# Kernel tuning notes

Hardware: AMD Instinct MI355X
Metric: run time of the kernel (lower is better)

Reference implementation:

```python
import jax, jax.numpy as jnp
import numpy as np

B, T, D_MODEL, N_HEADS = 2, 2048, 1024, 16
HEAD_DIM = D_MODEL // N_HEADS          # 64
CODE_SIZE = HEAD_DIM // 4              # 16


def setup_inputs() -> dict:
    key = jax.random.key(0)
    k1, k2, k3, k4 = jax.random.split(key, 4)
    x = jax.random.normal(k1, (B, T, D_MODEL), dtype=jnp.float32)
    # nn.Linear weights (out_features, in_features), fan-in init scale
    w_qkv = jax.random.normal(k2, (3 * D_MODEL, D_MODEL), dtype=jnp.float32) / np.sqrt(D_MODEL)
    w_out = jax.random.normal(k3, (D_MODEL, D_MODEL), dtype=jnp.float32) / np.sqrt(D_MODEL)
    fc_code = jax.random.normal(k4, (1, N_HEADS, CODE_SIZE, HEAD_DIM), dtype=jnp.float32)
    return {"x": x, "w_qkv": w_qkv, "w_out": w_out, "fc_code": fc_code}


def reference(x, w_qkv, w_out, fc_code):
    Bx, Tx, _ = x.shape
    scale = HEAD_DIM ** (-0.5)
    qkv = x @ w_qkv.T                                   # (B,T,3*d_model)
    # split_heads with Hs=head_dim on 3*d_model -> (B, 3*nH, T, Hs), then chunk on head axis
    qkv = qkv.reshape(Bx, Tx, 3 * N_HEADS, HEAD_DIM).transpose(0, 2, 1, 3)
    q, k, v = qkv[:, :N_HEADS], qkv[:, N_HEADS:2 * N_HEADS], qkv[:, 2 * N_HEADS:]
    code = fc_code[0]                                   # (nH, C, Hs)
    q = jnp.einsum('bhtd,hcd->bhtc', q, code) * scale   # (B,H,T,C)
    k = jnp.einsum('bhtd,hcd->bhtc', k, code) * scale
    q = jax.nn.softmax(q, axis=-1) * scale
    # causal branch (mask is None)
    k_exp = jnp.exp(k - jnp.max(k, axis=2, keepdims=True))       # (B,H,T,C)
    k_exp_cumsum = jnp.cumsum(k_exp, axis=2)                      # (B,H,T,C)
    kv_cumsum = jnp.cumsum(jnp.einsum('bhtc,bhtd->bhtcd', k_exp, v), axis=2)  # (B,H,T,C,D)
    kv = kv_cumsum / (k_exp_cumsum[..., None] + 1e-9)
    xo = jnp.einsum('bhtc,bhtcd->bhtd', q, kv)                    # (B,H,T,D)
    xo = xo.transpose(0, 2, 1, 3).reshape(Bx, Tx, D_MODEL)        # cat_heads
    return xo @ w_out.T
```

## Files before the change

### kernel.cpp

```cpp
#include <hip/hip_runtime.h>
#include <math.h>

#define B_    2
#define T_    2048
#define D_    1024
#define H_    16
#define HD_   64
#define C_    16
#define SCALE_ 0.125f
#define L_    128
#define NC_   16
#define QKP_  512

typedef __attribute__((ext_vector_type(8))) short short8;
typedef __attribute__((ext_vector_type(4))) float f32x4;

__device__ inline float b2f(uint32_t u16) {
    return __uint_as_float(u16 << 16);
}
__device__ inline ushort f2b(float f) {
    uint32_t u = __float_as_uint(f);
    return (ushort)((u + 0x7FFFu + ((u >> 16) & 1u)) >> 16);
}
__device__ inline uint32_t pack2(float a, float b) {
    return (uint32_t)f2b(a) | ((uint32_t)f2b(b) << 16);
}
__device__ inline void unpack2(uint32_t w, float& a, float& b) {
    a = b2f(w & 0xffffu); b = __uint_as_float(w & 0xffff0000u);
}
__device__ inline void unpack8(uint4 raw, float* dst) {
    unpack2(raw.x, dst[0], dst[1]);
    unpack2(raw.y, dst[2], dst[3]);
    unpack2(raw.z, dst[4], dst[5]);
    unpack2(raw.w, dst[6], dst[7]);
}
__device__ __forceinline__ void gll16(const ushort* g, ushort* l) {
    __builtin_amdgcn_global_load_lds(
        (const __attribute__((address_space(1))) void*)g,
        (__attribute__((address_space(3))) void*)l, 16, 0, 0);
}

__global__ __launch_bounds__(256)
void prep_inputs_kernel(const float* __restrict__ x, const float* __restrict__ w_qkv,
                        const float* __restrict__ w_out, const float* __restrict__ code,
                        ushort* __restrict__ xb, ushort* __restrict__ WallB,
                        ushort* __restrict__ WoB) {
    const int bid = blockIdx.x;
    if (bid < 3072) {
        const float* in;
        ushort* out;
        int i;
        if (bid < 2048) {
            in = x; out = xb;
            i = bid * 2048 + threadIdx.x * 8;
        } else {
            const int sub = bid - 2048;
            const int isW = sub >> 9;
            in = isW ? w_out : (w_qkv + (size_t)2048 * 1024);
            out = isW ? WoB : (WallB + (size_t)512 * 1024);
            i = (sub & 511) * 2048 + threadIdx.x * 8;
        }
        float4 a = *(const float4*)(in + i);
        float4 b = *(const float4*)(in + i + 4);
        uint4 o;
        o.x = pack2(a.x, a.y); o.y = pack2(a.z, a.w);
        o.z = pack2(b.x, b.y); o.w = pack2(b.z, b.w);
        *(uint4*)(out + i) = o;
    } else {
        const int sub = bid - 3072;
        const int isK = sub >> 6;
        const int h   = (sub >> 2) & 15;
        const int eq  = sub & 3;
        const int e   = eq * 256 + threadIdx.x;
        __shared__ __align__(16) float cs[C_][HD_];
        {
            float* csf = &cs[0][0];
            *(float4*)(csf + threadIdx.x * 4) =
                *(const float4*)(code + h * 1024 + threadIdx.x * 4);
        }
        __syncthreads();
        const float* wbase = w_qkv + ((size_t)(isK * D_ + h * HD_)) * D_ + e;
        float acc[C_];
        #pragma unroll
        for (int c = 0; c < C_; ++c) acc[c] = 0.f;
        #pragma unroll 4
        for (int db = 0; db < 16; ++db) {
            const float w0 = wbase[(size_t)(db * 4 + 0) * D_];
            const float w1 = wbase[(size_t)(db * 4 + 1) * D_];
            const float w2 = wbase[(size_t)(db * 4 + 2) * D_];
            const float w3 = wbase[(size_t)(db * 4 + 3) * D_];
            #pragma unroll
            for (int c = 0; c < C_; ++c) {
                float4 cv = *(const float4*)&cs[c][db * 4];
                acc[c] += w0 * cv.x; acc[c] += w1 * cv.y;
                acc[c] += w2 * cv.z; acc[c] += w3 * cv.w;
            }
        }
        ushort* outp = WallB + (size_t)(isK * 256 + h * 16) * D_ + e;
        #pragma unroll
        for (int c = 0; c < C_; ++c)
            outp[(size_t)c * D_] = f2b(acc[c] * SCALE_);
    }
}

template<int MODE>
__global__ __launch_bounds__(256)
void gemm_bf16_kernel(const ushort* __restrict__ A, const ushort* __restrict__ Bw,
                      void* __restrict__ Cv, ushort* __restrict__ vTout,
                      int M, int N, int K) {
    __shared__ ushort As[2][128 * 64];
    __shared__ ushort Bs[2][128 * 64];
    const int tid  = threadIdx.x;
    const int wave = tid >> 6;
    const int lane = tid & 63;
    const int wr = wave >> 1, wc = wave & 1;

    const int gx = gridDim.x;
    int f = blockIdx.y * gx + blockIdx.x;
    const int nwg = gx * gridDim.y;
    if ((nwg & 7) == 0) f = (f & 7) * (nwg >> 3) + (f >> 3);
    const int row0 = (f / gx) * 128;
    const int col0 = (f % gx) * 128;

    f32x4 acc[4][4];
    #pragma unroll
    for (int m = 0; m < 4; ++m)
        #pragma unroll
        for (int n = 0; n < 4; ++n) acc[m][n] = (f32x4){0.f, 0.f, 0.f, 0.f};

    const int srow = lane >> 3;
    const int kA   = ((lane & 7) ^ srow) << 3;
    const int lane15 = lane & 15;
    const int lhi    = lane >> 4;
    const int axor   = (lane15 & 7) << 4;

    const int NT = K >> 6;

    auto STAGE = [&](int buf, int kk) {
        #pragma unroll
        for (int i = 0; i < 8; ++i) {
            const int sg = wave * 8 + i;
            if (sg < 16) {
                const int r = sg * 8 + srow;
                gll16(A + (size_t)(row0 + r) * K + kk + kA, &As[buf][sg * 512]);
            } else {
                const int sb = sg - 16;
                const int r = sb * 8 + srow;
                gll16(Bw + (size_t)(col0 + r) * K + kk + kA, &Bs[buf][sb * 512]);
            }
        }
    };

    STAGE(0, 0);
    __syncthreads();

    for (int it = 0; it < NT; ++it) {
        const int cur = it & 1;
        if (it + 1 < NT) STAGE(cur ^ 1, (it + 1) << 6);
        const char* Ab = (const char*)As[cur];
        const char* Bb = (const char*)Bs[cur];
        #pragma unroll
        for (int s = 0; s < 2; ++s) {
            short8 af[4], bf[4];
            #pragma unroll
            for (int m = 0; m < 4; ++m) {
                const int r = wr * 64 + m * 16 + lane15;
                const int off = (r * 128 + s * 64 + lhi * 16) ^ axor;
                af[m] = *(const short8*)(Ab + off);
            }
            #pragma unroll
            for (int n = 0; n < 4; ++n) {
                const int r = wc * 64 + n * 16 + lane15;
                const int off = (r * 128 + s * 64 + lhi * 16) ^ axor;
                bf[n] = *(const short8*)(Bb + off);
            }
            #pragma unroll
            for (int m = 0; m < 4; ++m)
                #pragma unroll
                for (int n = 0; n < 4; ++n)
                    acc[m][n] = __builtin_amdgcn_mfma_f32_16x16x32_bf16(
                        af[m], bf[n], acc[m][n], 0, 0, 0);
        }
        __syncthreads();
    }

    if (MODE == 0) {
        float* C = (float*)Cv;
        #pragma unroll
        for (int m = 0; m < 4; ++m) {
            #pragma unroll
            for (int n = 0; n < 4; ++n) {
                const int row = row0 + wr * 64 + m * 16 + lhi * 4;
                const int col = col0 + wc * 64 + n * 16 + lane15;
                #pragma unroll
                for (int j = 0; j < 4; ++j)
                    C[(size_t)(row + j) * N + col] = acc[m][n][j];
            }
        }
    } else {
        char* pkB = (char*)As;
        if (col0 < 512) {
            #pragma unroll
            for (int m = 0; m < 4; ++m) {
                #pragma unroll
                for (int n = 0; n < 4; ++n) {
                    const int rl0 = wr * 64 + m * 16 + lhi * 4;
                    const int cl = wc * 64 + n * 16 + lane15;
                    #pragma unroll
                    for (int j = 0; j < 4; ++j) {
                        const int rl = rl0 + j;
                        *(ushort*)(pkB + ((rl * 256 + cl * 2) ^ ((rl & 7) << 4))) =
                            f2b(acc[m][n][j]);
                    }
                }
            }
            __syncthreads();
            ushort* C = (ushort*)Cv;
            #pragma unroll
            for (int i = 0; i < 8; ++i) {
                const int u = tid + i * 256;
                const int r = u >> 4, c8 = (u & 15) * 8;
                *(uint4*)(C + (size_t)(row0 + r) * QKP_ + col0 + c8) =
                    *(const uint4*)(pkB + ((r * 256 + c8 * 2) ^ ((r & 7) << 4)));
            }
        } else {
            #pragma unroll
            for (int m = 0; m < 4; ++m) {
                #pragma unroll
                for (int n = 0; n < 4; ++n) {
                    const int tl0 = wr * 64 + m * 16 + lhi * 4;
                    const int dl = wc * 64 + n * 16 + lane15;
                    const int off = (dl * 256 + tl0 * 2) ^ ((dl & 7) << 4);
                    *(uint2*)(pkB + off) = make_uint2(
                        pack2(acc[m][n][0], acc[m][n][1]),
                        pack2(acc[m][n][2], acc[m][n][3]));
                }
            }
            __syncthreads();
            const int h0  = (col0 - 512) >> 6;
            const int bb  = row0 >> 11;
            const int t0l = row0 & 2047;
            #pragma unroll
            for (int i = 0; i < 8; ++i) {
                const int u = tid + i * 256;
                const int d = u >> 4, t8 = (u & 15) * 8;
                const int hg = h0 + (d >> 6), dd = d & 63;
                const int off = (d * 256 + t8 * 2) ^ ((d & 7) << 4);
                *(uint4*)(vTout + ((size_t)((bb * 16 + hg) * 64 + dd)) * 2048 + t0l + t8) =
                    *(const uint4*)(pkB + off);
            }
        }
    }
}

__global__ __launch_bounds__(512)
void prep_attn_kernel(const ushort* __restrict__ qkcv, const ushort* __restrict__ vT,
                      float* __restrict__ ke_loc, float* __restrict__ kv_loc) {
    const int bid = blockIdx.x;
    const int chunk = bid & (NC_ - 1);
    const int bh = bid >> 4;
    const int b = bh >> 4, h = bh & 15;
    const int t0 = chunk * L_;
    const int tid = threadIdx.x;
    const int wave = tid >> 6, lane = tid & 63;
    const int l15 = lane & 15, lhi = lane >> 4;

    __shared__ __align__(16) ushort ke_bf[128 * 32];
    __shared__ __align__(16) ushort keTs[16 * 128];
    __shared__ __align__(16) ushort Vt_s[64 * 128];
    __shared__ float gsum[16][16];
    char* keB = (char*)ke_bf;
    char* keT = (char*)keTs;
    char* vtB = (char*)Vt_s;

    if (tid < 256) {
        const int t = tid >> 1, c0 = (tid & 1) * 8;
        uint4 raw = *(const uint4*)(qkcv + (size_t)(b * T_ + t0 + t) * QKP_ + 256 + h * C_ + c0);
        float f[8]; unpack8(raw, f);
        float ef[8];
        #pragma unroll
        for (int j = 0; j < 8; ++j) ef[j] = __expf(f[j]);
        uint4 o;
        o.x = pack2(ef[0], ef[1]); o.y = pack2(ef[2], ef[3]);
        o.z = pack2(ef[4], ef[5]); o.w = pack2(ef[6], ef[7]);
        const int swz = ((t >> 1) & 3) << 4;
        *(uint4*)(keB + ((t * 64 + c0 * 2) ^ swz)) = o;
        *(uint4*)(keB + ((t * 64 + 32 + c0 * 2) ^ swz)) = make_uint4(0, 0, 0, 0);
        #pragma unroll
        for (int j = 0; j < 8; ++j) {
            const int c = c0 + j;
            *(ushort*)(keT + (((c << 8) + (t << 1)) ^ (c << 4))) = f2b(ef[j]);
        }
    }
    {
        const int d = tid >> 3, qq = tid & 7;
        const ushort* src = vT + ((size_t)bh * 64 + d) * 2048 + t0 + qq * 16;
        const int swz = (d & 15) << 4;
        #pragma unroll
        for (int ii = 0; ii < 2; ++ii) {
            uint4 raw = *(const uint4*)(src + ii * 8);
            *(uint4*)(vtB + ((d * 256 + qq * 32 + ii * 16) ^ swz)) = raw;
        }
    }
    __syncthreads();

    if (wave < 4) {
        const int dt = wave;
        f32x4 kacc = (f32x4){0.f, 0.f, 0.f, 0.f};
        #pragma unroll
        for (int ks = 0; ks < 4; ++ks) {
            const int d = dt * 16 + l15;
            short8 av = *(const short8*)(vtB + ((d * 256 + ks * 64 + lhi * 16) ^ ((d & 15) << 4)));
            short8 bk = *(const short8*)(keT + (((l15 << 8) + ks * 64 + lhi * 16) ^ (l15 << 4)));
            kacc = __builtin_amdgcn_mfma_f32_16x16x32_bf16(av, bk, kacc, 0, 0, 0);
        }
        float* kvb = kv_loc + (size_t)bid * 1024;
        #pragma unroll
        for (int j = 0; j < 4; ++j)
            kvb[(dt * 16 + lhi * 4 + j) * 16 + l15] = kacc[j];
    } else {
        const int cc = tid & 15, g = (tid >> 4) & 15;
        float s = 0.f;
        #pragma unroll
        for (int u = 0; u < 8; ++u) {
            const int t = g * 8 + u;
            s += b2f(*(const ushort*)(keB + ((t * 64 + cc * 2) ^ (((t >> 1) & 3) << 4))));
        }
        gsum[cc][g] = s;
    }
    __syncthreads();
    if (tid < 16) {
        float s = 0.f;
        #pragma unroll
        for (int g = 0; g < 16; ++g) s += gsum[tid][g];
        ke_loc[(size_t)bid * C_ + tid] = s;
    }
}

__global__ __launch_bounds__(512)
void intra_kernel(const ushort* __restrict__ qkcv, const ushort* __restrict__ vT,
                  const float* __restrict__ ke_loc, const float* __restrict__ kv_loc,
                  ushort* __restrict__ xob) {
    const int bid = blockIdx.x;
    const int chunk = bid & (NC_ - 1);
    const int bh = bid >> 4;
    const int b = bh >> 4, h = bh & 15;
    const int t0 = chunk * L_;
    const int tid = threadIdx.x;
    const int wave = tid >> 6, lane = tid & 63;
    const int l15 = lane & 15, lhi = lane >> 4;

    __shared__ __align__(16) ushort ke_bf[128 * 32];
    __shared__ __align__(16) ushort qn_bf[128 * 32];
    __shared__ __align__(16) ushort Vt_s[64 * 128];
    __shared__ __align__(16) ushort Pl[128 * 128];
    __shared__ __align__(16) ushort S0t[64 * 32];
    __shared__ float kesum_s[128][16];
    __shared__ float gsum[16][16];
    __shared__ float e0s[16];

    char* keB = (char*)ke_bf;
    char* qnB = (char*)qn_bf;
    char* vtB = (char*)Vt_s;
    char* plB = (char*)Pl;
    char* s0B = (char*)S0t;

    if (tid < 256) {
        const int t = tid >> 1, c0 = (tid & 1) * 8;
        uint4 raw = *(const uint4*)(qkcv + (size_t)(b * T_ + t0 + t) * QKP_ + 256 + h * C_ + c0);
        float f[8]; unpack8(raw, f);
        uint4 o;
        o.x = pack2(__expf(f[0]), __expf(f[1]));
        o.y = pack2(__expf(f[2]), __expf(f[3]));
        o.z = pack2(__expf(f[4]), __expf(f[5]));
        o.w = pack2(__expf(f[6]), __expf(f[7]));
        const int swz = ((t >> 1) & 3) << 4;
        *(uint4*)(keB + ((t * 64 + c0 * 2) ^ swz)) = o;
        *(uint4*)(keB + ((t * 64 + 32 + c0 * 2) ^ swz)) = make_uint4(0, 0, 0, 0);
    }
    {
        const int d = tid >> 3, qq = tid & 7;
        const ushort* src = vT + ((size_t)bh * 64 + d) * 2048 + t0 + qq * 16;
        const int swz = (d & 15) << 4;
        #pragma unroll
        for (int ii = 0; ii < 2; ++ii) {
            uint4 raw = *(const uint4*)(src + ii * 8);
            *(uint4*)(vtB + ((d * 256 + qq * 32 + ii * 16) ^ swz)) = raw;
        }
    }
    if (tid < 16) {
        float s = 0.f;
        for (int ch = 0; ch < chunk; ++ch)
            s += ke_loc[(size_t)(bh * NC_ + ch) * C_ + tid];
        e0s[tid] = s;
    }
    __syncthreads();

    if (tid < 256) {
        const int d = tid >> 2;
        const int c0 = (tid & 3) * 4;
        const float* base = kv_loc + (size_t)(bh * NC_) * 1024 + d * 16 + c0;
        float s0 = 0.f, s1 = 0.f, s2 = 0.f, s3 = 0.f;
        for (int ch = 0; ch < chunk; ++ch) {
            float4 t4 = *(const float4*)(base + ch * 1024);
            s0 += t4.x; s1 += t4.y; s2 += t4.z; s3 += t4.w;
        }
        const int swz2 = ((d >> 1) & 3) << 4;
        *(uint2*)(s0B + ((d * 64 + c0 * 2) ^ swz2)) =
            make_uint2(pack2(s0, s1), pack2(s2, s3));
        *(uint2*)(s0B + ((d * 64 + 32 + (tid & 3) * 8) ^ swz2)) = make_uint2(0, 0);
    } else {
        const int cc = tid & 15, g = (tid >> 4) & 15;
        float s = 0.f;
        #pragma unroll
        for (int u = 0; u < 8; ++u) {
            const int t = g * 8 + u;
            s += b2f(*(const ushort*)(keB + ((t * 64 + cc * 2) ^ (((t >> 1) & 3) << 4))));
        }
        gsum[cc][g] = s;
    }
    __syncthreads();
    if (tid < 16) {
        float run = e0s[tid];
        #pragma unroll
        for (int g = 0; g < 16; ++g) { float tmp = gsum[tid][g]; gsum[tid][g] = run; run += tmp; }
    }
    __syncthreads();
    if (tid < 256) {
        const int cc = tid & 15, g = tid >> 4;
        float run = gsum[cc][g];
        #pragma unroll
        for (int u = 0; u < 8; ++u) {
            const int t = g * 8 + u;
            run += b2f(*(const ushort*)(keB + ((t * 64 + cc * 2) ^ (((t >> 1) & 3) << 4))));
            kesum_s[t][cc] = run;
        }
    }
    __syncthreads();

    if (tid < 128) {
        const int t = tid;
        const ushort* qrow = qkcv + (size_t)(b * T_ + t0 + t) * QKP_ + h * C_;
        float qv[16];
        uint4 r0 = *(const uint4*)qrow, r1 = *(const uint4*)(qrow + 8);
        unpack8(r0, qv); unpack8(r1, qv + 8);
        float m = qv[0];
        #pragma unroll
        for (int c = 1; c < 16; ++c) m = fmaxf(m, qv[c]);
        float sum = 0.f;
        #pragma unroll
        for (int c = 0; c < 16; ++c) { qv[c] = __expf(qv[c] - m); sum += qv[c]; }
        const float inv = SCALE_ / sum;
        #pragma unroll
        for (int c = 0; c < 16; ++c) qv[c] = qv[c] * inv / (kesum_s[t][c] + 1e-9f);
        uint4 o0, o1;
        o0.x = pack2(qv[0], qv[1]);   o0.y = pack2(qv[2], qv[3]);
        o0.z = pack2(qv[4], qv[5]);   o0.w = pack2(qv[6], qv[7]);
        o1.x = pack2(qv[8], qv[9]);   o1.y = pack2(qv[10], qv[11]);
        o1.z = pack2(qv[12], qv[13]); o1.w = pack2(qv[14], qv[15]);
        const int swz = ((t >> 1) & 3) << 4;
        *(uint4*)(qnB + ((t * 64) ^ swz)) = o0;
        *(uint4*)(qnB + ((t * 64 + 16) ^ swz)) = o1;
        *(uint4*)(qnB + ((t * 64 + 32) ^ swz)) = make_uint4(0, 0, 0, 0);
        *(uint4*)(qnB + ((t * 64 + 48) ^ swz)) = make_uint4(0, 0, 0, 0);
    }
    __syncthreads();

    {
        const int sb = wave;
        const int s_row = sb * 16 + l15;
        short8 af = *(const short8*)(keB + ((s_row * 64 + lhi * 16) ^ (((s_row >> 1) & 3) << 4)));
        #pragma unroll
        for (int tb = 0; tb < 8; ++tb) {
            f32x4 p = (f32x4){0.f, 0.f, 0.f, 0.f};
            if (tb >= sb) {
                const int t_col = tb * 16 + l15;
                short8 bf = *(const short8*)(qnB + ((t_col * 64 + lhi * 16) ^ (((t_col >> 1) & 3) << 4)));
                p = __builtin_amdgcn_mfma_f32_16x16x32_bf16(af, bf, p, 0, 0, 0);
                if (tb == sb) {
                    #pragma unroll
                    for (int j = 0; j < 4; ++j)
                        p[j] = (lhi * 4 + j > l15) ? 0.f : p[j];
                }
            }
            const int t_g = tb * 16 + l15;
            const int sbase = sb * 16 + lhi * 4;
            const int swz = (t_g & 15) << 4;
            *(uint32_t*)(plB + ((t_g * 256 + sbase * 2) ^ swz)) = pack2(p[0], p[1]);
            *(uint32_t*)(plB + ((t_g * 256 + sbase * 2 + 4) ^ swz)) = pack2(p[2], p[3]);
        }
    }
    __syncthreads();

    f32x4 acc4[4];
    #pragma unroll
    for (int dt = 0; dt < 4; ++dt) acc4[dt] = (f32x4){0.f, 0.f, 0.f, 0.f};

    {
        const int t_g = wave * 16 + l15;
        short8 aq = *(const short8*)(qnB + ((t_g * 64 + lhi * 16) ^ (((t_g >> 1) & 3) << 4)));
        #pragma unroll
        for (int dt = 0; dt < 4; ++dt) {
            const int d = dt * 16 + l15;
            short8 bs = *(const short8*)(s0B + ((d * 64 + lhi * 16) ^ (((d >> 1) & 3) << 4)));
            acc4[dt] = __builtin_amdgcn_mfma_f32_16x16x32_bf16(aq, bs, acc4[dt], 0, 0, 0);
        }
        const int pswz = (t_g & 15) << 4;
        #pragma unroll
        for (int kb = 0; kb < 4; ++kb) {
            short8 ap = *(const short8*)(plB + ((t_g * 256 + kb * 64 + lhi * 16) ^ pswz));
            #pragma unroll
            for (int dt = 0; dt < 4; ++dt) {
                const int d = dt * 16 + l15;
                short8 bv = *(const short8*)(vtB + ((d * 256 + kb * 64 + lhi * 16) ^ ((d & 15) << 4)));
                acc4[dt] = __builtin_amdgcn_mfma_f32_16x16x32_bf16(ap, bv, acc4[dt], 0, 0, 0);
            }
        }
    }

    __syncthreads();
    {
        ushort* ob = (ushort*)Pl;
        const int tl = wave * 16 + lhi * 4;
        #pragma unroll
        for (int dt = 0; dt < 4; ++dt) {
            const int d = dt * 16 + l15;
            #pragma unroll
            for (int j = 0; j < 4; ++j)
                ob[(tl + j) * 64 + d] = f2b(acc4[dt][j]);
        }
    }
    __syncthreads();
    {
        const ushort* ob = (const ushort*)Pl;
        #pragma unroll
        for (int i = 0; i < 2; ++i) {
            const int u = tid + i * 512;
            const int t = u >> 3, c8 = (u & 7) * 8;
            *(uint4*)(xob + (size_t)(b * T_ + t0 + t) * D_ + h * HD_ + c8) =
                *(const uint4*)(ob + t * 64 + c8);
        }
    }
}

extern "C" void kernel_launch(void* const* d_in, const int* in_sizes, int n_in,
                              void* d_out, int out_size, void* d_ws, size_t ws_size,
                              hipStream_t stream) {
    const float* x     = (const float*)d_in[0];
    const float* w_qkv = (const float*)d_in[1];
    const float* w_out = (const float*)d_in[2];
    const float* code  = (const float*)d_in[3];
    float* out = (float*)d_out;

    ushort* xb    = (ushort*)d_ws;
    ushort* WallB = xb + (size_t)4096 * 1024;
    ushort* WoB   = WallB + (size_t)1536 * 1024;
    ushort* qkcv  = WoB + (size_t)1024 * 1024;
    ushort* xob   = qkcv + (size_t)4096 * 512;
    ushort* vT    = xob + (size_t)4096 * 1024;
    float*  ke_loc = (float*)(vT + (size_t)32 * 64 * 2048);
    float*  kv_loc = ke_loc + 512 * 16;

    prep_inputs_kernel<<<3200, 256, 0, stream>>>(x, w_qkv, w_out, code, xb, WallB, WoB);

    gemm_bf16_kernel<2><<<dim3(12, 32), 256, 0, stream>>>(xb, WallB, qkcv, vT, 4096, 1536, 1024);

    prep_attn_kernel<<<512, 512, 0, stream>>>(qkcv, vT, ke_loc, kv_loc);
    intra_kernel<<<512, 512, 0, stream>>>(qkcv, vT, ke_loc, kv_loc, xob);

    gemm_bf16_kernel<0><<<dim3(8, 32), 256, 0, stream>>>(xob, WoB, out, nullptr, 4096, 1024, 1024);
}
```

Before: 74.90 us.

## Stage GEMM fp32 output through LDS and reuse exp(k) tile across kernels

The output GEMM now writes its fp32 accumulator tile into swizzled shared memory and then stores it to global with coalesced 16-byte rows instead of scattered 4-byte stores. The prep kernel also writes its bf16 exp(k) tile to a global scratch buffer, which the intra kernel loads directly rather than recomputing exp from qkcv. The intra kernel's serial per-channel prefix over group sums is replaced by each thread summing its prior groups, removing one barrier. The trade-offs are an extra LDS round trip and sync in the GEMM epilogue, plus extra global traffic for the exp(k) tile.

```diff
diff --git a/kernel.cpp b/kernel.cpp
--- a/kernel.cpp
+++ b/kernel.cpp
@@ -108,8 +108,9 @@
 void gemm_bf16_kernel(const ushort* __restrict__ A, const ushort* __restrict__ Bw,
                       void* __restrict__ Cv, ushort* __restrict__ vTout,
                       int M, int N, int K) {
-    __shared__ ushort As[2][128 * 64];
-    __shared__ ushort Bs[2][128 * 64];
+    __shared__ __align__(16) ushort SM[32768];
+    ushort* Asb = SM;
+    ushort* Bsb = SM + 16384;
     const int tid  = threadIdx.x;
     const int wave = tid >> 6;
     const int lane = tid & 63;
@@ -142,11 +143,11 @@
             const int sg = wave * 8 + i;
             if (sg < 16) {
                 const int r = sg * 8 + srow;
-                gll16(A + (size_t)(row0 + r) * K + kk + kA, &As[buf][sg * 512]);
+                gll16(A + (size_t)(row0 + r) * K + kk + kA, &Asb[buf * 8192 + sg * 512]);
             } else {
                 const int sb = sg - 16;
                 const int r = sb * 8 + srow;
-                gll16(Bw + (size_t)(col0 + r) * K + kk + kA, &Bs[buf][sb * 512]);
+                gll16(Bw + (size_t)(col0 + r) * K + kk + kA, &Bsb[buf * 8192 + sb * 512]);
             }
         }
     };
@@ -157,8 +158,8 @@
     for (int it = 0; it < NT; ++it) {
         const int cur = it & 1;
         if (it + 1 < NT) STAGE(cur ^ 1, (it + 1) << 6);
-        const char* Ab = (const char*)As[cur];
-        const char* Bb = (const char*)Bs[cur];
+        const char* Ab = (const char*)(Asb + cur * 8192);
+        const char* Bb = (const char*)(Bsb + cur * 8192);
         #pragma unroll
         for (int s = 0; s < 2; ++s) {
             short8 af[4], bf[4];
@@ -185,20 +186,31 @@
     }
 
     if (MODE == 0) {
+        char* pB = (char*)SM;
+        #pragma unroll
+        for (int m = 0; m < 4; ++m) {
+            #pragma unroll
+            for (int n = 0; n < 4; ++n) {
+                const int rl0 = wr * 64 + m * 16 + lhi * 4;
+                const int cl  = wc * 64 + n * 16 + lane15;
+                #pragma unroll
+                for (int j = 0; j < 4; ++j) {
+                    const int rl = rl0 + j;
+                    *(float*)(pB + ((rl * 512 + cl * 4) ^ ((rl & 7) << 4))) = acc[m][n][j];
+                }
+            }
+        }
+        __syncthreads();
         float* C = (float*)Cv;
         #pragma unroll
-        for (int m = 0; m < 4; ++m) {
-            #pragma unroll
-            for (int n = 0; n < 4; ++n) {
-                const int row = row0 + wr * 64 + m * 16 + lhi * 4;
-                const int col = col0 + wc * 64 + n * 16 + lane15;
-                #pragma unroll
-                for (int j = 0; j < 4; ++j)
-                    C[(size_t)(row + j) * N + col] = acc[m][n][j];
-            }
+        for (int i = 0; i < 16; ++i) {
+            const int idx = tid + i * 256;
+            const int r = idx >> 5, g = idx & 31;
+            *(uint4*)((char*)(C + (size_t)(row0 + r) * N + col0) + g * 16) =
+                *(const uint4*)(pB + ((r * 512 + g * 16) ^ ((r & 7) << 4)));
         }
     } else {
-        char* pkB = (char*)As;
+        char* pkB = (char*)SM;
         if (col0 < 512) {
             #pragma unroll
             for (int m = 0; m < 4; ++m) {
@@ -255,7 +267,8 @@
 
 __global__ __launch_bounds__(512)
 void prep_attn_kernel(const ushort* __restrict__ qkcv, const ushort* __restrict__ vT,
-                      float* __restrict__ ke_loc, float* __restrict__ kv_loc) {
+                      float* __restrict__ ke_loc, float* __restrict__ kv_loc,
+                      ushort* __restrict__ keg) {
     const int bid = blockIdx.x;
     const int chunk = bid & (NC_ - 1);
     const int bh = bid >> 4;
@@ -286,6 +299,9 @@
         const int swz = ((t >> 1) & 3) << 4;
         *(uint4*)(keB + ((t * 64 + c0 * 2) ^ swz)) = o;
         *(uint4*)(keB + ((t * 64 + 32 + c0 * 2) ^ swz)) = make_uint4(0, 0, 0, 0);
+        char* kb = (char*)(keg + (size_t)bid * 4096);
+        *(uint4*)(kb + ((t * 64 + c0 * 2) ^ swz)) = o;
+        *(uint4*)(kb + ((t * 64 + 32 + c0 * 2) ^ swz)) = make_uint4(0, 0, 0, 0);
         #pragma unroll
         for (int j = 0; j < 8; ++j) {
             const int c = c0 + j;
@@ -340,7 +356,7 @@
 __global__ __launch_bounds__(512)
 void intra_kernel(const ushort* __restrict__ qkcv, const ushort* __restrict__ vT,
                   const float* __restrict__ ke_loc, const float* __restrict__ kv_loc,
-                  ushort* __restrict__ xob) {
+                  const ushort* __restrict__ keg, ushort* __restrict__ xob) {
     const int bid = blockIdx.x;
     const int chunk = bid & (NC_ - 1);
     const int bh = bid >> 4;
@@ -365,19 +381,7 @@
     char* plB = (char*)Pl;
     char* s0B = (char*)S0t;
 
-    if (tid < 256) {
-        const int t = tid >> 1, c0 = (tid & 1) * 8;
-        uint4 raw = *(const uint4*)(qkcv + (size_t)(b * T_ + t0 + t) * QKP_ + 256 + h * C_ + c0);
-        float f[8]; unpack8(raw, f);
-        uint4 o;
-        o.x = pack2(__expf(f[0]), __expf(f[1]));
-        o.y = pack2(__expf(f[2]), __expf(f[3]));
-        o.z = pack2(__expf(f[4]), __expf(f[5]));
-        o.w = pack2(__expf(f[6]), __expf(f[7]));
-        const int swz = ((t >> 1) & 3) << 4;
-        *(uint4*)(keB + ((t * 64 + c0 * 2) ^ swz)) = o;
-        *(uint4*)(keB + ((t * 64 + 32 + c0 * 2) ^ swz)) = make_uint4(0, 0, 0, 0);
-    }
+    gll16(keg + (size_t)bid * 4096 + tid * 8, ke_bf + tid * 8);
     {
         const int d = tid >> 3, qq = tid & 7;
         const ushort* src = vT + ((size_t)bh * 64 + d) * 2048 + t0 + qq * 16;
@@ -420,15 +424,11 @@
         gsum[cc][g] = s;
     }
     __syncthreads();
-    if (tid < 16) {
-        float run = e0s[tid];
-        #pragma unroll
-        for (int g = 0; g < 16; ++g) { float tmp = gsum[tid][g]; gsum[tid][g] = run; run += tmp; }
-    }
-    __syncthreads();
+
     if (tid < 256) {
         const int cc = tid & 15, g = tid >> 4;
-        float run = gsum[cc][g];
+        float run = e0s[cc];
+        for (int g2 = 0; g2 < g; ++g2) run += gsum[cc][g2];
         #pragma unroll
         for (int u = 0; u < 8; ++u) {
             const int t = g * 8 + u;
@@ -560,13 +560,14 @@
     ushort* vT    = xob + (size_t)4096 * 1024;
     float*  ke_loc = (float*)(vT + (size_t)32 * 64 * 2048);
     float*  kv_loc = ke_loc + 512 * 16;
+    ushort* keg   = (ushort*)(kv_loc + (size_t)512 * 1024);
 
     prep_inputs_kernel<<<3200, 256, 0, stream>>>(x, w_qkv, w_out, code, xb, WallB, WoB);
 
     gemm_bf16_kernel<2><<<dim3(12, 32), 256, 0, stream>>>(xb, WallB, qkcv, vT, 4096, 1536, 1024);
 
-    prep_attn_kernel<<<512, 512, 0, stream>>>(qkcv, vT, ke_loc, kv_loc);
-    intra_kernel<<<512, 512, 0, stream>>>(qkcv, vT, ke_loc, kv_loc, xob);
+    prep_attn_kernel<<<512, 512, 0, stream>>>(qkcv, vT, ke_loc, kv_loc, keg);
+    intra_kernel<<<512, 512, 0, stream>>>(qkcv, vT, ke_loc, kv_loc, keg, xob);
 
     gemm_bf16_kernel<0><<<dim3(8, 32), 256, 0, stream>>>(xob, WoB, out, nullptr, 4096, 1024, 1024);
 }
```

New measurement: 78.84 us. 1.05x slower.
